# Kernel optimization log

Measured on AMD Instinct MI355X. Metric: run time of the kernel, lower is better.

## Reference

```python
import jax, jax.numpy as jnp
import numpy as np

# TT decomposition config (from Eff_TTEmbedding args in source)
P = (216, 216, 216)      # auto-factorized p_shapes for n=10,000,000 (216^3 >= n)
Q = (2, 4, 2)            # tt_q_shapes, prod = 16 = embedding_dim
R = (128, 128)           # tt_ranks
NUM_TABLES = 2
BATCH = 1024
NUM_EMB = 10_000_000


def setup_inputs() -> dict:
    key = jax.random.key(0)
    k0, k1, k2, k3 = jax.random.split(key, 4)
    # sparse indices per TT table: [n_tables, batch]
    lS_i = jax.random.randint(k3, (NUM_TABLES, BATCH), 0, NUM_EMB, dtype=jnp.int64)
    # TT cores, weight_dist='uniform'
    core0 = jax.random.uniform(k0, (NUM_TABLES, P[0], Q[0] * R[0]), dtype=jnp.float32, minval=-0.01, maxval=0.01)
    core1 = jax.random.uniform(k1, (NUM_TABLES, P[1], R[0] * Q[1] * R[1]), dtype=jnp.float32, minval=-0.01, maxval=0.01)
    core2 = jax.random.uniform(k2, (NUM_TABLES, P[2], R[1] * Q[2]), dtype=jnp.float32, minval=-0.01, maxval=0.01)
    return {"lS_i": lS_i, "core0": core0, "core1": core1, "core2": core2}


def _tt_lookup(idx, c0, c1, c2):
    """TT embedding lookup for one table. idx: [B] int; returns [B, prod(Q)]."""
    B = idx.shape[0]
    # mixed-radix decomposition of flat index into (i0, i1, i2)
    i0 = idx // (P[1] * P[2])
    i1 = (idx // P[2]) % P[1]
    i2 = idx % P[2]
    # gather TT core slices (the memory-bound irregular access)
    A = c0[i0].reshape(B, Q[0], R[0])            # [B, 2, 128]
    Bm = c1[i1].reshape(B, R[0], Q[1] * R[1])    # [B, 128, 512]
    C = c2[i2].reshape(B, R[1], Q[2])            # [B, 128, 2]
    # chained small matmuls along TT ranks
    AB = jnp.einsum('bqr,brs->bqs', A, Bm).reshape(B, Q[0] * Q[1], R[1])  # [B, 8, 128]
    out = jnp.einsum('bqr,brs->bqs', AB, C)      # [B, 8, 2]
    return out.reshape(B, Q[0] * Q[1] * Q[2])    # [B, 16]


def reference(lS_i, core0, core1, core2):
    # per-table dispatch (forward returns one embedding bag per TT table)
    return jax.vmap(_tt_lookup)(lS_i, core0, core1, core2)  # [n_tables, B, 16]
```

## Files before the change

kernel.cpp:

```cpp
#include <hip/hip_runtime.h>


#define NGROUPS 432
#define NLOOK   2048

__global__ __launch_bounds__(512) void tt_prep(const int* __restrict__ idx32,
                                               int* __restrict__ w) {
    __shared__ int cnt[NGROUPS];
    __shared__ int scan[512];
    __shared__ int cursor[NGROUPS];
    const int tid = threadIdx.x;

    for (int i = tid; i < NGROUPS; i += 512) cnt[i] = 0;
    __syncthreads();

    const bool is64 = (idx32[1] == 0) & (idx32[3] == 0) &
                      (idx32[5] == 0) & (idx32[7] == 0);

    int grp[4];
#pragma unroll
    for (int j = 0; j < 4; ++j) {
        const int id = tid + j * 512;
        const unsigned idx = is64 ? (unsigned)((const long long*)idx32)[id]
                                  : (unsigned)idx32[id];
        const unsigned i0  = idx / 46656u;
        const unsigned rem = idx - i0 * 46656u;
        const unsigned i1  = rem / 216u;
        const unsigned i2  = rem - i1 * 216u;
        const int table = id >> 10;
        grp[j] = table * 216 + (int)i1;
        w[2912 + id] = (int)((i0 << 16) | i2);
        atomicAdd(&cnt[grp[j]], 1);
    }
    __syncthreads();

    scan[tid] = (tid < NGROUPS) ? cnt[tid] : 0;
    __syncthreads();
    for (int off = 1; off < 512; off <<= 1) {
        const int v   = scan[tid];
        const int add = (tid >= off) ? scan[tid - off] : 0;
        __syncthreads();
        scan[tid] = v + add;
        __syncthreads();
    }
    if (tid < NGROUPS) {
        const int st = scan[tid] - cnt[tid];
        w[tid]        = st;
        w[432 + tid]  = cnt[tid];
        cursor[tid]   = st;
    }
    __syncthreads();

#pragma unroll
    for (int j = 0; j < 4; ++j) {
        const int id  = tid + j * 512;
        const int pos = atomicAdd(&cursor[grp[j]], 1);
        w[864 + pos] = id;
    }
}

__global__ __launch_bounds__(128) void tt_main(
    const float* __restrict__ c0,
    const float* __restrict__ c1,
    const float* __restrict__ c2,
    const int* __restrict__ w,
    float* __restrict__ out)
{
    const int g = blockIdx.x;
    const int h = blockIdx.y;
    const int cs = blockIdx.z;
    const int m = w[432 + g];
    if (m <= cs * 8) return;
    const int s0    = w[g];
    const int table = g / 216;
    const int i1    = g - table * 216;

    const int tid = threadIdx.x;
    const int wv  = tid >> 6;
    const int tl  = tid & 63;

    __shared__ float comb[4096];
    float4* comb4 = (float4*)comb;
    __shared__ int s_id[8];
    __shared__ int s_aux[8];

    const float4* b4 = (const float4*)(c1 + (((size_t)table * 216 + i1) << 16))
                       + (h * 64 + tl) + (size_t)(wv * 64) * 128;

    for (int base = cs * 8; base < m; base += 16) {
        const int cl = min(8, m - base);
        __syncthreads();
        if (tid < 8) {
            const bool ok = tid < cl;
            const int id  = ok ? w[864 + s0 + base + tid] : 0;
            s_id[tid]  = id;
            s_aux[tid] = ok ? w[2912 + id] : -1;
        }
        __syncthreads();

#pragma unroll
        for (int l = 0; l < 8; ++l) {
            const int aux = s_aux[l];
            const float* ar = c0 + ((size_t)table * 216 + (aux >> 16)) * 256;
#pragma unroll
            for (int k = 0; k < 2; ++k) {
                const int e = tid + 128 * k;
                comb[l * 256 + e] = (aux >= 0) ? ar[((e & 1) << 7) + (e >> 1)] : 0.f;
            }
        }
        __syncthreads();

        float4 acc[8][2];
#pragma unroll
        for (int l = 0; l < 8; ++l) {
            acc[l][0] = make_float4(0.f, 0.f, 0.f, 0.f);
            acc[l][1] = make_float4(0.f, 0.f, 0.f, 0.f);
        }

#pragma unroll 8
        for (int rr = 0; rr < 64; ++rr) {
            const float4 bv = b4[(size_t)rr * 128];
            const int r = wv * 64 + rr;
#pragma unroll
            for (int l = 0; l < 8; ++l) {
                const float2 av = ((const float2*)(comb + l * 256))[r];
                acc[l][0].x += av.x * bv.x; acc[l][0].y += av.x * bv.y;
                acc[l][0].z += av.x * bv.z; acc[l][0].w += av.x * bv.w;
                acc[l][1].x += av.y * bv.x; acc[l][1].y += av.y * bv.y;
                acc[l][1].z += av.y * bv.z; acc[l][1].w += av.y * bv.w;
            }
        }

        __syncthreads();
        if (wv == 1) {
#pragma unroll
            for (int l = 0; l < 8; ++l) {
                comb4[(l * 2 + 0) * 64 + tl] = acc[l][0];
                comb4[(l * 2 + 1) * 64 + tl] = acc[l][1];
            }
        }
        __syncthreads();

        if (wv == 0) {
            const int q1 = 2 * h + (tl >> 5);
            const int r1 = (tl & 31) * 4;
#pragma unroll
            for (int l = 0; l < 8; ++l) {
                const float4 t0 = comb4[(l * 2 + 0) * 64 + tl];
                const float4 t1 = comb4[(l * 2 + 1) * 64 + tl];
                acc[l][0].x += t0.x; acc[l][0].y += t0.y;
                acc[l][0].z += t0.z; acc[l][0].w += t0.w;
                acc[l][1].x += t1.x; acc[l][1].y += t1.y;
                acc[l][1].z += t1.z; acc[l][1].w += t1.w;
                if (l < cl) {
                    const int aux = s_aux[l];
                    const float* crow = c2 + ((size_t)table * 216 + (aux & 0xffff)) * 256;
                    const float4 cA = *(const float4*)(crow + r1 * 2);
                    const float4 cB = *(const float4*)(crow + r1 * 2 + 4);
                    float p00 = acc[l][0].x*cA.x + acc[l][0].y*cA.z + acc[l][0].z*cB.x + acc[l][0].w*cB.z;
                    float p01 = acc[l][0].x*cA.y + acc[l][0].y*cA.w + acc[l][0].z*cB.y + acc[l][0].w*cB.w;
                    float p10 = acc[l][1].x*cA.x + acc[l][1].y*cA.z + acc[l][1].z*cB.x + acc[l][1].w*cB.z;
                    float p11 = acc[l][1].x*cA.y + acc[l][1].y*cA.w + acc[l][1].z*cB.y + acc[l][1].w*cB.w;
#pragma unroll
                    for (int mm = 16; mm >= 1; mm >>= 1) {
                        p00 += __shfl_xor(p00, mm);
                        p01 += __shfl_xor(p01, mm);
                        p10 += __shfl_xor(p10, mm);
                        p11 += __shfl_xor(p11, mm);
                    }
                    if ((tl & 31) == 0) {
                        float* o = out + (size_t)s_id[l] * 16;
                        o[q1 * 2 + 0]     = p00;
                        o[q1 * 2 + 1]     = p01;
                        o[8 + q1 * 2 + 0] = p10;
                        o[8 + q1 * 2 + 1] = p11;
                    }
                }
            }
        }
    }
}

extern "C" void kernel_launch(void* const* d_in, const int* in_sizes, int n_in,
                              void* d_out, int out_size, void* d_ws, size_t ws_size,
                              hipStream_t stream) {
    const int*   idx = (const int*)d_in[0];
    const float* c0  = (const float*)d_in[1];
    const float* c1  = (const float*)d_in[2];
    const float* c2  = (const float*)d_in[3];
    float* out = (float*)d_out;
    int* w = (int*)d_ws;

    tt_prep<<<dim3(1), dim3(512), 0, stream>>>(idx, w);
    tt_main<<<dim3(NGROUPS, 2, 2), dim3(128), 0, stream>>>(c0, c1, c2, w, out);
}
```

Baseline: 183.7 us.

## Split main kernel across four q1 slices and use wave-shuffle scan in prep

The main kernel's grid grows from 2 to 4 y-slices, so each block handles one q1 column pair with float2 loads of core1 instead of float4. This halves the per-thread accumulators and LDS use and doubles the block count for latency hiding. The c0 staging becomes a coalesced read with a transposed LDS write, and the c2 contraction now uses a full 64-lane shuffle reduction. The prep kernel swaps its LDS Hillis-Steele scan, which needed many block barriers, for a wavefront shuffle scan plus per-wave totals. The cost is more blocks, each reloading the c0 rows and scheduling separately.

```diff
diff --git a/kernel.cpp b/kernel.cpp
--- a/kernel.cpp
+++ b/kernel.cpp
@@ -7,9 +7,11 @@
 __global__ __launch_bounds__(512) void tt_prep(const int* __restrict__ idx32,
                                                int* __restrict__ w) {
     __shared__ int cnt[NGROUPS];
-    __shared__ int scan[512];
+    __shared__ int wtot[8];
     __shared__ int cursor[NGROUPS];
-    const int tid = threadIdx.x;
+    const int tid  = threadIdx.x;
+    const int lane = tid & 63;
+    const int wv   = tid >> 6;
 
     for (int i = tid; i < NGROUPS; i += 512) cnt[i] = 0;
     __syncthreads();
@@ -34,20 +36,22 @@
     }
     __syncthreads();
 
-    scan[tid] = (tid < NGROUPS) ? cnt[tid] : 0;
+    const int v = (tid < NGROUPS) ? cnt[tid] : 0;
+    int s = v;
+#pragma unroll
+    for (int d = 1; d < 64; d <<= 1) {
+        const int t = __shfl_up(s, d);
+        if (lane >= d) s += t;
+    }
+    if (lane == 63) wtot[wv] = s;
     __syncthreads();
-    for (int off = 1; off < 512; off <<= 1) {
-        const int v   = scan[tid];
-        const int add = (tid >= off) ? scan[tid - off] : 0;
-        __syncthreads();
-        scan[tid] = v + add;
-        __syncthreads();
-    }
+    int off = 0;
+    for (int i = 0; i < wv; ++i) off += wtot[i];
     if (tid < NGROUPS) {
-        const int st = scan[tid] - cnt[tid];
-        w[tid]        = st;
-        w[432 + tid]  = cnt[tid];
-        cursor[tid]   = st;
+        const int st = s + off - v;
+        w[tid]       = st;
+        w[432 + tid] = v;
+        cursor[tid]  = st;
     }
     __syncthreads();
 
@@ -66,8 +70,8 @@
     const int* __restrict__ w,
     float* __restrict__ out)
 {
-    const int g = blockIdx.x;
-    const int h = blockIdx.y;
+    const int g  = blockIdx.x;
+    const int q  = blockIdx.y;
     const int cs = blockIdx.z;
     const int m = w[432 + g];
     if (m <= cs * 8) return;
@@ -76,16 +80,17 @@
     const int i1    = g - table * 216;
 
     const int tid = threadIdx.x;
-    const int wv  = tid >> 6;
+    const int rh  = tid >> 6;
     const int tl  = tid & 63;
 
-    __shared__ float comb[4096];
-    float4* comb4 = (float4*)comb;
+    __shared__ float lds[2048];
+    float2* lds2 = (float2*)lds;
     __shared__ int s_id[8];
     __shared__ int s_aux[8];
 
-    const float4* b4 = (const float4*)(c1 + (((size_t)table * 216 + i1) << 16))
-                       + (h * 64 + tl) + (size_t)(wv * 64) * 128;
+    const float2* b2 = (const float2*)(c1 + (((size_t)(table * 216 + i1)) << 16))
+                       + (size_t)rh * 64 * 256 + (q * 64 + tl);
+    const float* c0t = c0 + (size_t)table * 216 * 256;
 
     for (int base = cs * 8; base < m; base += 16) {
         const int cl = min(8, m - base);
@@ -94,86 +99,77 @@
             const bool ok = tid < cl;
             const int id  = ok ? w[864 + s0 + base + tid] : 0;
             s_id[tid]  = id;
-            s_aux[tid] = ok ? w[2912 + id] : -1;
+            s_aux[tid] = ok ? w[2912 + id] : 0;
         }
         __syncthreads();
 
 #pragma unroll
         for (int l = 0; l < 8; ++l) {
-            const int aux = s_aux[l];
-            const float* ar = c0 + ((size_t)table * 216 + (aux >> 16)) * 256;
+            const float* ar = c0t + (size_t)(s_aux[l] >> 16) * 256;
 #pragma unroll
             for (int k = 0; k < 2; ++k) {
                 const int e = tid + 128 * k;
-                comb[l * 256 + e] = (aux >= 0) ? ar[((e & 1) << 7) + (e >> 1)] : 0.f;
+                lds[l * 256 + 2 * (e & 127) + (e >> 7)] = ar[e];
             }
         }
         __syncthreads();
 
-        float4 acc[8][2];
+        float2 acc[8][2];
 #pragma unroll
         for (int l = 0; l < 8; ++l) {
-            acc[l][0] = make_float4(0.f, 0.f, 0.f, 0.f);
-            acc[l][1] = make_float4(0.f, 0.f, 0.f, 0.f);
+            acc[l][0] = make_float2(0.f, 0.f);
+            acc[l][1] = make_float2(0.f, 0.f);
         }
 
 #pragma unroll 8
         for (int rr = 0; rr < 64; ++rr) {
-            const float4 bv = b4[(size_t)rr * 128];
-            const int r = wv * 64 + rr;
+            const float2 bv = b2[(size_t)rr * 256];
+            const int r = rh * 64 + rr;
 #pragma unroll
             for (int l = 0; l < 8; ++l) {
-                const float2 av = ((const float2*)(comb + l * 256))[r];
+                const float2 av = lds2[l * 128 + r];
                 acc[l][0].x += av.x * bv.x; acc[l][0].y += av.x * bv.y;
-                acc[l][0].z += av.x * bv.z; acc[l][0].w += av.x * bv.w;
                 acc[l][1].x += av.y * bv.x; acc[l][1].y += av.y * bv.y;
-                acc[l][1].z += av.y * bv.z; acc[l][1].w += av.y * bv.w;
             }
         }
 
         __syncthreads();
-        if (wv == 1) {
+        if (rh == 1) {
 #pragma unroll
             for (int l = 0; l < 8; ++l) {
-                comb4[(l * 2 + 0) * 64 + tl] = acc[l][0];
-                comb4[(l * 2 + 1) * 64 + tl] = acc[l][1];
+                lds2[(l * 2 + 0) * 64 + tl] = acc[l][0];
+                lds2[(l * 2 + 1) * 64 + tl] = acc[l][1];
             }
         }
         __syncthreads();
 
-        if (wv == 0) {
-            const int q1 = 2 * h + (tl >> 5);
-            const int r1 = (tl & 31) * 4;
+        if (rh == 0) {
 #pragma unroll
             for (int l = 0; l < 8; ++l) {
-                const float4 t0 = comb4[(l * 2 + 0) * 64 + tl];
-                const float4 t1 = comb4[(l * 2 + 1) * 64 + tl];
-                acc[l][0].x += t0.x; acc[l][0].y += t0.y;
-                acc[l][0].z += t0.z; acc[l][0].w += t0.w;
-                acc[l][1].x += t1.x; acc[l][1].y += t1.y;
-                acc[l][1].z += t1.z; acc[l][1].w += t1.w;
+                const float2 t0 = lds2[(l * 2 + 0) * 64 + tl];
+                const float2 t1 = lds2[(l * 2 + 1) * 64 + tl];
+                const float a0x = acc[l][0].x + t0.x, a0y = acc[l][0].y + t0.y;
+                const float a1x = acc[l][1].x + t1.x, a1y = acc[l][1].y + t1.y;
                 if (l < cl) {
-                    const int aux = s_aux[l];
-                    const float* crow = c2 + ((size_t)table * 216 + (aux & 0xffff)) * 256;
-                    const float4 cA = *(const float4*)(crow + r1 * 2);
-                    const float4 cB = *(const float4*)(crow + r1 * 2 + 4);
-                    float p00 = acc[l][0].x*cA.x + acc[l][0].y*cA.z + acc[l][0].z*cB.x + acc[l][0].w*cB.z;
-                    float p01 = acc[l][0].x*cA.y + acc[l][0].y*cA.w + acc[l][0].z*cB.y + acc[l][0].w*cB.w;
-                    float p10 = acc[l][1].x*cA.x + acc[l][1].y*cA.z + acc[l][1].z*cB.x + acc[l][1].w*cB.z;
-                    float p11 = acc[l][1].x*cA.y + acc[l][1].y*cA.w + acc[l][1].z*cB.y + acc[l][1].w*cB.w;
+                    const float* crow = c2 + (size_t)(table * 216 + (s_aux[l] & 0xffff)) * 256;
+                    const float4 cv = *(const float4*)(crow + 4 * tl);
+                    float p00 = a0x * cv.x + a0y * cv.z;
+                    float p01 = a0x * cv.y + a0y * cv.w;
+                    float p10 = a1x * cv.x + a1y * cv.z;
+                    float p11 = a1x * cv.y + a1y * cv.w;
 #pragma unroll
-                    for (int mm = 16; mm >= 1; mm >>= 1) {
+                    for (int mm = 32; mm >= 1; mm >>= 1) {
                         p00 += __shfl_xor(p00, mm);
                         p01 += __shfl_xor(p01, mm);
                         p10 += __shfl_xor(p10, mm);
                         p11 += __shfl_xor(p11, mm);
                     }
-                    if ((tl & 31) == 0) {
+                    if (tl == 0) {
                         float* o = out + (size_t)s_id[l] * 16;
-                        o[q1 * 2 + 0]     = p00;
-                        o[q1 * 2 + 1]     = p01;
-                        o[8 + q1 * 2 + 0] = p10;
-                        o[8 + q1 * 2 + 1] = p11;
+                        o[q * 2 + 0]     = p00;
+                        o[q * 2 + 1]     = p01;
+                        o[8 + q * 2 + 0] = p10;
+                        o[8 + q * 2 + 1] = p11;
                     }
                 }
             }
@@ -192,5 +188,5 @@
     int* w = (int*)d_ws;
 
     tt_prep<<<dim3(1), dim3(512), 0, stream>>>(idx, w);
-    tt_main<<<dim3(NGROUPS, 2, 2), dim3(128), 0, stream>>>(c0, c1, c2, w, out);
+    tt_main<<<dim3(NGROUPS, 4, 2), dim3(128), 0, stream>>>(c0, c1, c2, w, out);
 }
```

Result: no change. 182.8 us (-0.4%).
